# Performance work log

Hardware: AMD Instinct MI355X
Metric: run time of the kernel (lower is better)

The kernel has to match this reference:

```python
import jax, jax.numpy as jnp
import numpy as np

N_NODES = 50000
N_EDGES = 1600000
DIM = 128          # input_dim == hidden_dim == embed_dim
N_LAYERS = 5
NEG_SLOPE = 0.2    # PyG GATv2Conv default


def setup_inputs() -> dict:
    key = jax.random.key(0)
    ks = jax.random.split(key, 8)
    s = 1.0 / np.sqrt(DIM)
    x = jax.random.normal(ks[0], (N_NODES, DIM), dtype=jnp.float32)
    edge_index = jax.random.randint(ks[1], (2, N_EDGES), 0, N_NODES, dtype=jnp.int64)
    # stacked per-layer params (all dims are 128 so layers stack cleanly)
    Wl = jax.random.normal(ks[2], (N_LAYERS, DIM, DIM), dtype=jnp.float32) * s
    bl = jax.random.normal(ks[3], (N_LAYERS, DIM), dtype=jnp.float32) * 0.01
    Wr = jax.random.normal(ks[4], (N_LAYERS, DIM, DIM), dtype=jnp.float32) * s
    br = jax.random.normal(ks[5], (N_LAYERS, DIM), dtype=jnp.float32) * 0.01
    att = jax.random.normal(ks[6], (N_LAYERS, DIM), dtype=jnp.float32) * s
    bias = jax.random.normal(ks[7], (N_LAYERS, DIM), dtype=jnp.float32) * 0.01
    return {"x": x, "edge_index": edge_index, "Wl": Wl, "bl": bl,
            "Wr": Wr, "br": br, "att": att, "bias": bias}


def _gatv2_layer(x, src, dst, Wl, bl, Wr, br, att, bias):
    # x: [N, D]; src/dst: [E'] (self loops already appended)
    n = x.shape[0]
    xl = x @ Wl + bl                      # [N, D]  (source transform; also the message)
    xr = x @ Wr + br                      # [N, D]  (target transform)
    # per-edge GATv2 score: att . LeakyReLU(xl[src] + xr[dst])
    e = jax.nn.leaky_relu(xl[src] + xr[dst], NEG_SLOPE) @ att   # [E']
    # numerically stable segment-softmax over incoming edges of each dst node
    m = jax.ops.segment_max(e, dst, num_segments=n)
    m = jnp.where(jnp.isfinite(m), m, jnp.zeros_like(m))
    p = jnp.exp(e - m[dst])
    z = jax.ops.segment_sum(p, dst, num_segments=n)
    alpha = p / jnp.maximum(z[dst], jnp.asarray(1e-16, p.dtype))  # [E']
    out = jax.ops.segment_sum(alpha[:, None] * xl[src], dst, num_segments=n)
    return out + bias


def reference(x, edge_index, Wl, bl, Wr, br, att, bias):
    n = x.shape[0]
    # PyG GATv2Conv default add_self_loops=True; edges identical across layers -> append once
    loop = jnp.arange(n, dtype=edge_index.dtype)
    src = jnp.concatenate([edge_index[0], loop])
    dst = jnp.concatenate([edge_index[1], loop])
    h = x
    for i in range(N_LAYERS):
        h = _gatv2_layer(h, src, dst, Wl[i], bl[i], Wr[i], br[i], att[i], bias[i])
        if i < N_LAYERS - 1:
            h = jax.nn.relu(h)
    # global_mean_pool with batch=None -> mean over all nodes, shape [1, embed_dim]
    return jnp.mean(h, axis=0, keepdims=True)
```

## Files before the change

kernel.cpp:

```cpp
#include <hip/hip_runtime.h>
#include <hip/hip_bf16.h>

#define N_NODES 50000
#define N_EDGES 1600000
#define DIM 128
#define N_LAYERS 5
#define NEG 0.2f

#define NBKT 196
#define BCAP_A 9472
#define PBLK 98
#define EPB 16384
#define SEGCAP 12288
#define SENT N_NODES
#define LOG2E 1.4426950408889634f

typedef unsigned short u16;
typedef unsigned char u8;
typedef unsigned int u32;
using short8 = __attribute__((ext_vector_type(8))) short;
using f32x4  = __attribute__((ext_vector_type(4))) float;
typedef float f32x2 __attribute__((ext_vector_type(2)));

union FragU { uint4 u; short8 s; };

__device__ __forceinline__ f32x2 bf2v(u32 u) {
    union { u32 i; float f; } lo, hi;
    lo.i = u << 16;
    hi.i = u & 0xffff0000u;
    f32x2 r; r.x = lo.f; r.y = hi.f;
    return r;
}
__device__ __forceinline__ u16 f2bf(float f) {
    union { float f; u32 u; } v; v.f = f;
    u32 r = v.u + 0x7fffu + ((v.u >> 16) & 1u);
    return (u16)(r >> 16);
}
__device__ __forceinline__ u32 cvtpk(float a, float b) {
    u32 r;
    asm("v_cvt_pk_bf16_f32 %0, %1, %2" : "=v"(r) : "v"(a), "v"(b));
    return r;
}
__device__ __forceinline__ u32 pk2(float a, float b) {
    return (u32)f2bf(a) | ((u32)f2bf(b) << 16);
}
__device__ __forceinline__ int clampi(int v) {
    v = (v < 0) ? 0 : v;
    return (v >= N_NODES) ? (N_NODES - 1) : v;
}
template<int CTRL>
__device__ __forceinline__ float rradd(float v) {
    int t = __builtin_amdgcn_update_dpp(0, __float_as_int(v), CTRL, 0xF, 0xF, true);
    return v + __int_as_float(t);
}

__global__ void k_probe(const int* __restrict__ ei32, int* __restrict__ flags,
                        int* __restrict__ bcnt) {
    __shared__ int cnt;
    int t = threadIdx.x;
    if (t == 0) cnt = 0;
    __syncthreads();
    if (ei32[2 * t + 1] == 0) atomicAdd(&cnt, 1);
    if (t < NBKT) bcnt[t] = 0;
    __syncthreads();
    if (t == 0) flags[0] = (cnt >= 255) ? 1 : 0;
}

__device__ __forceinline__ int ldidx(const void* ei, long long i, int m64) {
    int v = m64 ? (int)(((const long long*)ei)[i]) : ((const int*)ei)[i];
    return clampi(v);
}

__global__ void k_cvt_x(const float* __restrict__ x, u16* __restrict__ xb) {
    int i = blockIdx.x * 256 + threadIdx.x;
    float2 v = *(const float2*)(x + (size_t)i * 2);
    ((u32*)xb)[i] = cvtpk(v.x, v.y);
}

__global__ void k_cvt_w(const float* __restrict__ Wl, const float* __restrict__ Wr,
                        uint4* __restrict__ Wtg) {
    int id = blockIdx.x * 256 + threadIdx.x;
    if (id >= N_LAYERS * 16 * 256) return;
    int l = id >> 12;
    int rem = id & 4095;
    int kc = rem >> 8;
    int n = rem & 255;
    const float* W = (n < 128) ? (Wl + (size_t)l * DIM * DIM + n)
                               : (Wr + (size_t)l * DIM * DIM + (n - 128));
    u16 c[8];
#pragma unroll
    for (int j = 0; j < 8; ++j) c[j] = f2bf(W[(size_t)(kc * 8 + j) * DIM]);
    uint4 o;
    o.x = (u32)c[0] | ((u32)c[1] << 16);
    o.y = (u32)c[2] | ((u32)c[3] << 16);
    o.z = (u32)c[4] | ((u32)c[5] << 16);
    o.w = (u32)c[6] | ((u32)c[7] << 16);
    Wtg[(size_t)l * 4096 + n * 16 + (kc ^ (n & 15))] = o;
}

__global__ __launch_bounds__(1024) void k_part(
    const void* __restrict__ ei, const int* __restrict__ flags,
    int* __restrict__ bcnt, u32* __restrict__ bpk)
{
    __shared__ u32 ebuf[EPB];
    __shared__ u8  bkb[EPB];
    __shared__ int lh[NBKT];
    __shared__ int lb[NBKT + 1];
    __shared__ int gst[NBKT];
    __shared__ int sc[256];

    const int tid = threadIdx.x;
    const int m64 = flags[0];
    const long long e0 = (long long)blockIdx.x * EPB;

    for (int i = tid; i < NBKT; i += 1024) lh[i] = 0;
    __syncthreads();

    u32 pay[16];
    u32 meta[16];
    int nv = 0;
#pragma unroll
    for (int i = 0; i < 16; ++i) {
        long long e = e0 + i * 1024 + tid;
        if (e < N_EDGES) {
            int s = ldidx(ei, e, m64);
            int d = ldidx(ei, (long long)N_EDGES + e, m64);
            int b = d >> 8;
            int rank = atomicAdd(&lh[b], 1);
            pay[i] = (u32)s | ((u32)(d & 255) << 16);
            meta[i] = (u32)b | ((u32)rank << 8);
            nv = i + 1;
        }
    }
    __syncthreads();

    if (tid < 256) sc[tid] = (tid < NBKT) ? lh[tid] : 0;
    __syncthreads();
    for (int off = 1; off < 256; off <<= 1) {
        int v = 0;
        if (tid < 256 && tid >= off) v = sc[tid - off];
        __syncthreads();
        if (tid < 256) sc[tid] += v;
        __syncthreads();
    }
    if (tid < NBKT) lb[tid] = sc[tid] - lh[tid];
    if (tid == 0) lb[NBKT] = 0;
    if (tid < NBKT) gst[tid] = atomicAdd(&bcnt[tid], lh[tid]);
    __syncthreads();

#pragma unroll
    for (int i = 0; i < 16; ++i) {
        if (i < nv) {
            int b = (int)(meta[i] & 255);
            int rank = (int)(meta[i] >> 8);
            int p = lb[b] + rank;
            ebuf[p] = pay[i];
            bkb[p] = (u8)b;
        }
    }
    __syncthreads();

    int total = (e0 + EPB <= N_EDGES) ? EPB : (int)(N_EDGES - e0);
    for (int i = tid; i < total; i += 1024) {
        int b = (int)bkb[i];
        int off = gst[b] + (i - lb[b]);
        if (off < BCAP_A)
            bpk[(size_t)b * BCAP_A + off] = ebuf[i];
    }
}

__global__ __launch_bounds__(256) void k_deg(
    const u32* __restrict__ bpk, const int* __restrict__ bcnt,
    const void* __restrict__ ei, const int* __restrict__ flags,
    int* __restrict__ row_off, int* __restrict__ btot)
{
    __shared__ int dh[256];
    __shared__ int sc[256];
    int b = blockIdx.x;
    int tid = threadIdx.x;
    dh[tid] = 0;
    __syncthreads();
    int cnt = bcnt[b];
    if (cnt <= BCAP_A) {
        for (int i = tid; i < cnt; i += 256)
            atomicAdd(&dh[(bpk[(size_t)b * BCAP_A + i] >> 16) & 255], 1);
    } else {
        int m64 = flags[0];
        for (long long e = tid; e < N_EDGES; e += 256) {
            int d = ldidx(ei, (long long)N_EDGES + e, m64);
            if ((d >> 8) == b) atomicAdd(&dh[d & 255], 1);
        }
    }
    __syncthreads();
    int d = b * 256 + tid;
    int v = 0;
    if (d < N_NODES) {
        v = (dh[tid] + 1 + 3) & ~3;
        if (v < 16) v = 16;
    }
    sc[tid] = v;
    __syncthreads();
    for (int off = 1; off < 256; off <<= 1) {
        int t = (tid >= off) ? sc[tid - off] : 0;
        __syncthreads();
        sc[tid] += t;
        __syncthreads();
    }
    if (d < N_NODES) row_off[d] = sc[tid] - v;
    if (tid == 255) btot[b] = sc[255];
}

__global__ void k_bscan(const int* __restrict__ btot, int* __restrict__ boff,
                        int* __restrict__ row_off) {
    __shared__ int sc[256];
    int tid = threadIdx.x;
    int v = (tid < NBKT) ? btot[tid] : 0;
    sc[tid] = v;
    __syncthreads();
    for (int off = 1; off < 256; off <<= 1) {
        int t = (tid >= off) ? sc[tid - off] : 0;
        __syncthreads();
        sc[tid] += t;
        __syncthreads();
    }
    if (tid < NBKT) boff[tid] = sc[tid] - v;
    if (tid == NBKT - 1) row_off[N_NODES] = sc[tid];
}

__global__ __launch_bounds__(256) void k_scat(
    const u32* __restrict__ bpk, const int* __restrict__ bcnt,
    int* __restrict__ row_off, const int* __restrict__ boff,
    const int* __restrict__ btot, u32* __restrict__ col,
    const void* __restrict__ ei, const int* __restrict__ flags)
{
    __shared__ u32 stage[SEGCAP];
    __shared__ int cur[256];
    int b = blockIdx.x;
    int tid = threadIdx.x;
    int d_lo = b * 256;
    int d_hi = d_lo + 256; if (d_hi > N_NODES) d_hi = N_NODES;
    int base0 = boff[b];
    int seglen = btot[b];
    if (seglen > SEGCAP) seglen = SEGCAP;

    int d = d_lo + tid;
    int rloc = 0;
    int ext = 0;
    if (d < d_hi) {
        rloc = row_off[d];
        ext = (d + 1 < d_hi) ? row_off[d + 1] : btot[b];
        if (ext > SEGCAP) ext = SEGCAP;
        if (rloc < SEGCAP) stage[rloc] = (u32)d * 256u;
        cur[tid] = rloc + 1;
    }
    __syncthreads();

    int cnt = bcnt[b];
    if (cnt <= BCAP_A) {
        for (int i = tid; i < cnt; i += 256) {
            u32 p = bpk[(size_t)b * BCAP_A + i];
            int pos = atomicAdd(&cur[(p >> 16) & 255], 1);
            if (pos < SEGCAP) stage[pos] = (p & 0xffffu) * 256u;
        }
    } else {
        int m64 = flags[0];
        for (long long e = tid; e < N_EDGES; e += 256) {
            int dd = ldidx(ei, (long long)N_EDGES + e, m64);
            if ((dd >> 8) == b) {
                int s = ldidx(ei, e, m64);
                int pos = atomicAdd(&cur[dd & 255], 1);
                if (pos < SEGCAP) stage[pos] = (u32)s * 256u;
            }
        }
    }
    __syncthreads();
    if (d < d_hi) {
        for (int i = cur[tid]; i < ext; ++i) stage[i] = (u32)SENT * 256u;
    }
    __syncthreads();
    for (int i = tid; i < seglen; i += 256)
        col[base0 + i] = stage[i];
    if (d < d_hi) row_off[d] = base0 + rloc;
}

__global__ __launch_bounds__(256) void k_mm(
    const u16* __restrict__ hb,
    const uint4* __restrict__ Wtg,
    const float* __restrict__ bl, const float* __restrict__ br,
    const float* __restrict__ att,
    u16* __restrict__ xlb,
    u16* __restrict__ xrb)
{
    __shared__ uint4 wsh[4096];
    const int tid = threadIdx.x;
#pragma unroll
    for (int i = 0; i < 16; ++i) wsh[tid + i * 256] = Wtg[tid + i * 256];

    const int wave = tid >> 6, lane = tid & 63;
    const int q = lane >> 4, nn = lane & 15;
    const int mA = blockIdx.x * 64 + wave * 16 + nn;

    FragU afr[4];
    const uint4 az = make_uint4(0, 0, 0, 0);
#pragma unroll
    for (int s = 0; s < 4; ++s)
        afr[s].u = (mA < N_NODES)
                 ? *(const uint4*)(hb + (size_t)mA * DIM + s * 32 + q * 8)
                 : az;
    __syncthreads();

    f32x4 acc[16];
#pragma unroll
    for (int i = 0; i < 16; ++i) acc[i] = (f32x4){0.f, 0.f, 0.f, 0.f};

#pragma unroll
    for (int s = 0; s < 4; ++s) {
#pragma unroll
        for (int nt = 0; nt < 16; ++nt) {
            int n = nt * 16 + nn;
            int kc = s * 4 + q;
            FragU b;
            b.u = wsh[n * 16 + (kc ^ (n & 15))];
            acc[nt] = __builtin_amdgcn_mfma_f32_16x16x32_bf16(b.s, afr[s].s, acc[nt], 0, 0, 0);
        }
    }

    const bool valid = (mA < N_NODES);
#pragma unroll
    for (int nt = 0; nt < 16; ++nt) {
        int n0 = nt * 16 + q * 4;
        bool isL = (n0 < 128);
        const float* bp = isL ? (bl + n0) : (br + (n0 - 128));
        float4 bv = *(const float4*)bp;
        float v0 = acc[nt][0] + bv.x;
        float v1 = acc[nt][1] + bv.y;
        float v2 = acc[nt][2] + bv.z;
        float v3 = acc[nt][3] + bv.w;
        uint2 o;
        o.x = cvtpk(v0, v1);
        o.y = cvtpk(v2, v3);
        if (valid) {
            u16* dst = isL ? (xlb + (size_t)mA * DIM + n0)
                           : (xrb + (size_t)mA * DIM + (n0 - 128));
            *(uint2*)dst = o;
        }
    }

    if (blockIdx.x == 0 && tid < DIM) {
        float s = att[tid];
        xlb[(size_t)SENT * DIM + tid] = f2bf(s >= 0.f ? -10000.f : 10000.f);
    }
}

#define PROC(U) do {                                                          \
    f32x2 x01 = bf2v((U).x), x23 = bf2v((U).y);                               \
    f32x2 x45 = bf2v((U).z), x67 = bf2v((U).w);                               \
    f32x2 z01 = x01 + xr01, z23 = x23 + xr23;                                 \
    f32x2 z45 = x45 + xr45, z67 = x67 + xr67;                                 \
    z01 = __builtin_elementwise_max(z01, z01 * negv);                         \
    z23 = __builtin_elementwise_max(z23, z23 * negv);                         \
    z45 = __builtin_elementwise_max(z45, z45 * negv);                         \
    z67 = __builtin_elementwise_max(z67, z67 * negv);                         \
    f32x2 pp2 = at01 * z01;                                                   \
    pp2 = at23 * z23 + pp2;                                                   \
    pp2 = at45 * z45 + pp2;                                                   \
    pp2 = at67 * z67 + pp2;                                                   \
    float pp = pp2.x + pp2.y;                                                 \
    pp = rradd<0x121>(pp);                                                    \
    pp = rradd<0x122>(pp);                                                    \
    pp = rradd<0x124>(pp);                                                    \
    pp = rradd<0x128>(pp);                                                    \
    float w_ = __builtin_amdgcn_exp2f(pp);                                    \
    lsum += w_;                                                               \
    f32x2 wv; wv.x = w_; wv.y = w_;                                           \
    ac01 = wv * x01 + ac01; ac23 = wv * x23 + ac23;                           \
    ac45 = wv * x45 + ac45; ac67 = wv * x67 + ac67;                           \
} while (0)

#define LDQ(U, Q) do {                                                        \
    u32 ob_ = __shfl(off, ((Q) << 2) + g, 64);                                \
    (U) = *(const uint4*)(xbp + (size_t)(ob_ + dofs));                        \
} while (0)

template <int RELU>
__global__ __launch_bounds__(64) void k_edge(
    const u16* __restrict__ xlb, const u16* __restrict__ xrb,
    const int* __restrict__ row_off, const u32* __restrict__ col,
    const float* __restrict__ att, const float* __restrict__ bias,
    u16* __restrict__ hout)
{
    const int node = blockIdx.x;
    const int lane = threadIdx.x & 63;
    const int g = lane >> 4;
    const int t = lane & 15;

    const int d0 = t * 8;
    const u32 dofs = (u32)(t << 4);
    const char* xbp = (const char*)xlb;

    uint4 xru = *(const uint4*)(xrb + (size_t)node * DIM + d0);
    f32x2 xr01 = bf2v(xru.x), xr23 = bf2v(xru.y), xr45 = bf2v(xru.z), xr67 = bf2v(xru.w);
    float2 a0 = *(const float2*)(att + d0);
    float2 a1 = *(const float2*)(att + d0 + 2);
    float2 a2 = *(const float2*)(att + d0 + 4);
    float2 a3 = *(const float2*)(att + d0 + 6);
    f32x2 at01, at23, at45, at67;
    at01.x = a0.x * LOG2E; at01.y = a0.y * LOG2E;
    at23.x = a1.x * LOG2E; at23.y = a1.y * LOG2E;
    at45.x = a2.x * LOG2E; at45.y = a2.y * LOG2E;
    at67.x = a3.x * LOG2E; at67.y = a3.y * LOG2E;
    f32x2 negv; negv.x = NEG; negv.y = NEG;

    const int beg = __builtin_amdgcn_readfirstlane(row_off[node]);
    const int end = __builtin_amdgcn_readfirstlane(row_off[node + 1]);
    const int n = end - beg;
    const int nreg = (n < 64) ? n : 64;
    const int nq = nreg >> 2;

    u32 off = col[beg + lane];

    f32x2 ac01, ac23, ac45, ac67;
    ac01.x = ac01.y = ac23.x = ac23.y = 0.f;
    ac45.x = ac45.y = ac67.x = ac67.y = 0.f;
    float lsum = 0.f;

    uint4 u0, u1, u2, u3;
    LDQ(u0, 0); LDQ(u1, 1); LDQ(u2, 2); LDQ(u3, 3);

    int q = 0;
    for (; q + 8 <= nq; q += 4) {
        PROC(u0); LDQ(u0, q + 4);
        PROC(u1); LDQ(u1, q + 5);
        PROC(u2); LDQ(u2, q + 6);
        PROC(u3); LDQ(u3, q + 7);
    }
    PROC(u0); if (q + 4 < nq) LDQ(u0, q + 4);
    PROC(u1); if (q + 5 < nq) LDQ(u1, q + 5);
    PROC(u2); if (q + 6 < nq) LDQ(u2, q + 6);
    PROC(u3); if (q + 7 < nq) LDQ(u3, q + 7);
    q += 4;
    if (q     < nq) PROC(u0);
    if (q + 1 < nq) PROC(u1);
    if (q + 2 < nq) PROC(u2);

    for (int j = beg + 64 + g; j < end; j += 4) {
        u32 ob_ = col[j];
        uint4 u = *(const uint4*)(xbp + (size_t)(ob_ + dofs));
        PROC(u);
    }

    float accv[8] = {ac01.x, ac01.y, ac23.x, ac23.y, ac45.x, ac45.y, ac67.x, ac67.y};
#pragma unroll
    for (int i = 0; i < 8; ++i) {
        accv[i] += __shfl_xor(accv[i], 16, 64);
        accv[i] += __shfl_xor(accv[i], 32, 64);
    }
    lsum += __shfl_xor(lsum, 16, 64);
    lsum += __shfl_xor(lsum, 32, 64);

    if (g == 0) {
        float inv = 1.f / fmaxf(lsum, 1e-16f);
        float4 b0 = *(const float4*)(bias + d0);
        float4 b1 = *(const float4*)(bias + d0 + 4);
        float o0 = accv[0] * inv + b0.x;
        float o1 = accv[1] * inv + b0.y;
        float o2 = accv[2] * inv + b0.z;
        float o3 = accv[3] * inv + b0.w;
        float o4 = accv[4] * inv + b1.x;
        float o5 = accv[5] * inv + b1.y;
        float o6 = accv[6] * inv + b1.z;
        float o7 = accv[7] * inv + b1.w;
        if (RELU) {
            o0 = fmaxf(o0, 0.f); o1 = fmaxf(o1, 0.f);
            o2 = fmaxf(o2, 0.f); o3 = fmaxf(o3, 0.f);
            o4 = fmaxf(o4, 0.f); o5 = fmaxf(o5, 0.f);
            o6 = fmaxf(o6, 0.f); o7 = fmaxf(o7, 0.f);
        }
        uint4 o;
        o.x = cvtpk(o0, o1);
        o.y = cvtpk(o2, o3);
        o.z = cvtpk(o4, o5);
        o.w = cvtpk(o6, o7);
        *(uint4*)(hout + (size_t)node * DIM + d0) = o;
    }
}

__global__ void k_mean_part(const u16* __restrict__ hb, float* __restrict__ part) {
    int d = threadIdx.x;
    int b = blockIdx.x;
    int n0 = b * 200;
    float s = 0.f;
    for (int i = 0; i < 200; ++i) {
        union { u32 i; float f; } v;
        v.i = (u32)hb[(size_t)(n0 + i) * DIM + d] << 16;
        s += v.f;
    }
    part[b * DIM + d] = s;
}

__global__ void k_mean_final(const float* __restrict__ part, float* __restrict__ out) {
    int d = threadIdx.x;
    float s = 0.f;
    for (int b = 0; b < 250; ++b) s += part[b * DIM + d];
    out[d] = s * (1.f / (float)N_NODES);
}

extern "C" void kernel_launch(void* const* d_in, const int* in_sizes, int n_in,
                              void* d_out, int out_size, void* d_ws, size_t ws_size,
                              hipStream_t stream) {
    int ix, iei, iWl, ibl, iWr, ibr, iatt, ibias;
    if (in_sizes[0] == N_NODES * DIM) {
        ix = 0; iei = 1; iWl = 2; ibl = 3; iWr = 4; ibr = 5; iatt = 6; ibias = 7;
    } else {
        iWl = 0; iWr = 1; iatt = 2; ibias = 3; ibl = 4; ibr = 5; iei = 6; ix = 7;
    }
    const float* x    = (const float*)d_in[ix];
    const void*  ei   = d_in[iei];
    const float* Wl   = (const float*)d_in[iWl];
    const float* bl   = (const float*)d_in[ibl];
    const float* Wr   = (const float*)d_in[iWr];
    const float* br   = (const float*)d_in[ibr];
    const float* att  = (const float*)d_in[iatt];
    const float* bias = (const float*)d_in[ibias];
    float* out = (float*)d_out;

    char* w = (char*)d_ws;
    float* part = (float*)w;      w += (size_t)256 * DIM * 4;
    uint4* Wtg = (uint4*)w;       w += (size_t)N_LAYERS * 4096 * 16;
    u16* xb  = (u16*)w;           w += (size_t)N_NODES * DIM * 2;
    u16* hb  = (u16*)w;           w += (size_t)N_NODES * DIM * 2;
    u16* xlb = (u16*)w;           w += (size_t)(N_NODES + 1) * DIM * 2;
    u16* xrb = (u16*)w;           w += (size_t)N_NODES * DIM * 2;
    int* row_off = (int*)w;       w += (size_t)(N_NODES + 4) * 4;
    int* flags = (int*)w;         w += 64;
    int* bcnt = (int*)w;          w += (size_t)(NBKT + 4) * 4;
    int* btot = (int*)w;          w += (size_t)(NBKT + 4) * 4;
    int* boff = (int*)w;          w += (size_t)(NBKT + 4) * 4;
    u32* bpk = (u32*)w;           w += (size_t)NBKT * BCAP_A * 4;
    u32* col = (u32*)w;           w += (size_t)(N_EDGES + 8 * N_NODES + 64) * 4;

    k_probe<<<1, 256, 0, stream>>>((const int*)ei, flags, bcnt);
    k_cvt_x<<<(N_NODES * DIM / 2 + 255) / 256, 256, 0, stream>>>(x, xb);
    k_cvt_w<<<(N_LAYERS * 4096 + 255) / 256, 256, 0, stream>>>(Wl, Wr, Wtg);
    k_part<<<PBLK, 1024, 0, stream>>>(ei, flags, bcnt, bpk);
    k_deg<<<NBKT, 256, 0, stream>>>(bpk, bcnt, ei, flags, row_off, btot);
    k_bscan<<<1, 256, 0, stream>>>(btot, boff, row_off);
    k_scat<<<NBKT, 256, 0, stream>>>(bpk, bcnt, row_off, boff, btot, col, ei, flags);

    const int mm_grid = (N_NODES + 63) / 64;

    for (int layer = 0; layer < N_LAYERS; ++layer) {
        const uint4* Wp = Wtg + (size_t)layer * 4096;
        const float* blp = bl + (size_t)layer * DIM;
        const float* brp = br + (size_t)layer * DIM;
        const float* ap  = att + (size_t)layer * DIM;
        const float* bp  = bias + (size_t)layer * DIM;

        const u16* hin = (layer == 0) ? xb : hb;
        k_mm<<<mm_grid, 256, 0, stream>>>(hin, Wp, blp, brp, ap, xlb, xrb);

        if (layer < N_LAYERS - 1)
            k_edge<1><<<N_NODES, 64, 0, stream>>>(xlb, xrb, row_off, col, ap, bp, hb);
        else
            k_edge<0><<<N_NODES, 64, 0, stream>>>(xlb, xrb, row_off, col, ap, bp, hb);
    }

    k_mean_part<<<250, 128, 0, stream>>>(hb, part);
    k_mean_final<<<1, 128, 0, stream>>>(part, out);
}
```

Baseline: 510.7 us.

## Double rows per GEMM block, halve partition chunk, vectorize mean reduction

The node-transform GEMM now computes two 16-row tiles per wave (128 rows per block), so each weight fragment loaded from LDS feeds two MFMAs and the per-block weight staging is spread over twice the work. The edge partition kernel uses twice as many blocks with half the edges each, raising parallelism for that preprocessing step. The mean-pool partial kernel switches to 16-byte vector loads with shuffle and LDS reduction over 400-row chunks. The larger GEMM tile doubles the accumulator registers, which may lower occupancy, and the GEMM grid halves.

```diff
diff --git a/kernel.cpp b/kernel.cpp
--- a/kernel.cpp
+++ b/kernel.cpp
@@ -9,8 +9,8 @@
 
 #define NBKT 196
 #define BCAP_A 9472
-#define PBLK 98
-#define EPB 16384
+#define PBLK 196
+#define EPB 8192
 #define SEGCAP 12288
 #define SENT N_NODES
 #define LOG2E 1.4426950408889634f
@@ -40,9 +40,6 @@
     u32 r;
     asm("v_cvt_pk_bf16_f32 %0, %1, %2" : "=v"(r) : "v"(a), "v"(b));
     return r;
-}
-__device__ __forceinline__ u32 pk2(float a, float b) {
-    return (u32)f2bf(a) | ((u32)f2bf(b) << 16);
 }
 __device__ __forceinline__ int clampi(int v) {
     v = (v < 0) ? 0 : v;
@@ -116,11 +113,11 @@
     for (int i = tid; i < NBKT; i += 1024) lh[i] = 0;
     __syncthreads();
 
-    u32 pay[16];
-    u32 meta[16];
+    u32 pay[8];
+    u32 meta[8];
     int nv = 0;
 #pragma unroll
-    for (int i = 0; i < 16; ++i) {
+    for (int i = 0; i < 8; ++i) {
         long long e = e0 + i * 1024 + tid;
         if (e < N_EDGES) {
             int s = ldidx(ei, e, m64);
@@ -149,7 +146,7 @@
     __syncthreads();
 
 #pragma unroll
-    for (int i = 0; i < 16; ++i) {
+    for (int i = 0; i < 8; ++i) {
         if (i < nv) {
             int b = (int)(meta[i] & 255);
             int rank = (int)(meta[i] >> 8);
@@ -298,20 +295,26 @@
 
     const int wave = tid >> 6, lane = tid & 63;
     const int q = lane >> 4, nn = lane & 15;
-    const int mA = blockIdx.x * 64 + wave * 16 + nn;
-
-    FragU afr[4];
+    const int mA0 = blockIdx.x * 128 + wave * 16 + nn;
+    const int mA1 = mA0 + 64;
+
+    FragU a0[4], a1[4];
     const uint4 az = make_uint4(0, 0, 0, 0);
 #pragma unroll
-    for (int s = 0; s < 4; ++s)
-        afr[s].u = (mA < N_NODES)
-                 ? *(const uint4*)(hb + (size_t)mA * DIM + s * 32 + q * 8)
-                 : az;
-    __syncthreads();
-
-    f32x4 acc[16];
-#pragma unroll
-    for (int i = 0; i < 16; ++i) acc[i] = (f32x4){0.f, 0.f, 0.f, 0.f};
+    for (int s = 0; s < 4; ++s) {
+        a0[s].u = (mA0 < N_NODES)
+                ? *(const uint4*)(hb + (size_t)mA0 * DIM + s * 32 + q * 8) : az;
+        a1[s].u = (mA1 < N_NODES)
+                ? *(const uint4*)(hb + (size_t)mA1 * DIM + s * 32 + q * 8) : az;
+    }
+    __syncthreads();
+
+    f32x4 acc0[16], acc1[16];
+#pragma unroll
+    for (int i = 0; i < 16; ++i) {
+        acc0[i] = (f32x4){0.f, 0.f, 0.f, 0.f};
+        acc1[i] = (f32x4){0.f, 0.f, 0.f, 0.f};
+    }
 
 #pragma unroll
     for (int s = 0; s < 4; ++s) {
@@ -321,28 +324,32 @@
             int kc = s * 4 + q;
             FragU b;
             b.u = wsh[n * 16 + (kc ^ (n & 15))];
-            acc[nt] = __builtin_amdgcn_mfma_f32_16x16x32_bf16(b.s, afr[s].s, acc[nt], 0, 0, 0);
-        }
-    }
-
-    const bool valid = (mA < N_NODES);
+            acc0[nt] = __builtin_amdgcn_mfma_f32_16x16x32_bf16(b.s, a0[s].s, acc0[nt], 0, 0, 0);
+            acc1[nt] = __builtin_amdgcn_mfma_f32_16x16x32_bf16(b.s, a1[s].s, acc1[nt], 0, 0, 0);
+        }
+    }
+
+    const bool v0 = (mA0 < N_NODES);
+    const bool v1 = (mA1 < N_NODES);
 #pragma unroll
     for (int nt = 0; nt < 16; ++nt) {
         int n0 = nt * 16 + q * 4;
         bool isL = (n0 < 128);
         const float* bp = isL ? (bl + n0) : (br + (n0 - 128));
         float4 bv = *(const float4*)bp;
-        float v0 = acc[nt][0] + bv.x;
-        float v1 = acc[nt][1] + bv.y;
-        float v2 = acc[nt][2] + bv.z;
-        float v3 = acc[nt][3] + bv.w;
-        uint2 o;
-        o.x = cvtpk(v0, v1);
-        o.y = cvtpk(v2, v3);
-        if (valid) {
-            u16* dst = isL ? (xlb + (size_t)mA * DIM + n0)
-                           : (xrb + (size_t)mA * DIM + (n0 - 128));
-            *(uint2*)dst = o;
+        uint2 o0, o1;
+        o0.x = cvtpk(acc0[nt][0] + bv.x, acc0[nt][1] + bv.y);
+        o0.y = cvtpk(acc0[nt][2] + bv.z, acc0[nt][3] + bv.w);
+        o1.x = cvtpk(acc1[nt][0] + bv.x, acc1[nt][1] + bv.y);
+        o1.y = cvtpk(acc1[nt][2] + bv.z, acc1[nt][3] + bv.w);
+        int nc = isL ? n0 : (n0 - 128);
+        if (v0) {
+            u16* dst = (isL ? xlb : xrb) + (size_t)mA0 * DIM + nc;
+            *(uint2*)dst = o0;
+        }
+        if (v1) {
+            u16* dst = (isL ? xlb : xrb) + (size_t)mA1 * DIM + nc;
+            *(uint2*)dst = o1;
         }
     }
 
@@ -485,23 +492,48 @@
     }
 }
 
-__global__ void k_mean_part(const u16* __restrict__ hb, float* __restrict__ part) {
-    int d = threadIdx.x;
+__global__ __launch_bounds__(256) void k_mean_part(const u16* __restrict__ hb,
+                                                   float* __restrict__ part) {
+    __shared__ float sh[4][16][8];
+    int t = threadIdx.x;
     int b = blockIdx.x;
-    int n0 = b * 200;
-    float s = 0.f;
-    for (int i = 0; i < 200; ++i) {
-        union { u32 i; float f; } v;
-        v.i = (u32)hb[(size_t)(n0 + i) * DIM + d] << 16;
-        s += v.f;
-    }
-    part[b * DIM + d] = s;
+    int c0 = (t & 15) * 8;
+    int rl = t >> 4;
+    int n0 = b * 400;
+    float acc[8] = {0.f, 0.f, 0.f, 0.f, 0.f, 0.f, 0.f, 0.f};
+    for (int i = 0; i < 25; ++i) {
+        int r = n0 + rl + i * 16;
+        uint4 v = *(const uint4*)(hb + (size_t)r * DIM + c0);
+        f32x2 p0 = bf2v(v.x), p1 = bf2v(v.y), p2 = bf2v(v.z), p3 = bf2v(v.w);
+        acc[0] += p0.x; acc[1] += p0.y;
+        acc[2] += p1.x; acc[3] += p1.y;
+        acc[4] += p2.x; acc[5] += p2.y;
+        acc[6] += p3.x; acc[7] += p3.y;
+    }
+#pragma unroll
+    for (int i = 0; i < 8; ++i) {
+        acc[i] += __shfl_xor(acc[i], 16, 64);
+        acc[i] += __shfl_xor(acc[i], 32, 64);
+    }
+    int wave = t >> 6;
+    if ((t & 63) < 16) {
+#pragma unroll
+        for (int i = 0; i < 8; ++i) sh[wave][t & 15][i] = acc[i];
+    }
+    __syncthreads();
+    if (t < 16) {
+#pragma unroll
+        for (int i = 0; i < 8; ++i) {
+            float s = sh[0][t][i] + sh[1][t][i] + sh[2][t][i] + sh[3][t][i];
+            part[b * DIM + t * 8 + i] = s;
+        }
+    }
 }
 
 __global__ void k_mean_final(const float* __restrict__ part, float* __restrict__ out) {
     int d = threadIdx.x;
     float s = 0.f;
-    for (int b = 0; b < 250; ++b) s += part[b * DIM + d];
+    for (int b = 0; b < 125; ++b) s += part[b * DIM + d];
     out[d] = s * (1.f / (float)N_NODES);
 }
 
@@ -547,7 +579,7 @@
     k_bscan<<<1, 256, 0, stream>>>(btot, boff, row_off);
     k_scat<<<NBKT, 256, 0, stream>>>(bpk, bcnt, row_off, boff, btot, col, ei, flags);
 
-    const int mm_grid = (N_NODES + 63) / 64;
+    const int mm_grid = (N_NODES + 127) / 128;
 
     for (int layer = 0; layer < N_LAYERS; ++layer) {
         const uint4* Wp = Wtg + (size_t)layer * 4096;
@@ -565,6 +597,6 @@
             k_edge<0><<<N_NODES, 64, 0, stream>>>(xlb, xrb, row_off, col, ap, bp, hb);
     }
 
-    k_mean_part<<<250, 128, 0, stream>>>(hb, part);
+    k_mean_part<<<125, 256, 0, stream>>>(hb, part);
     k_mean_final<<<1, 128, 0, stream>>>(part, out);
 }
```

Result: faster. 485.7 us (-4.9%).
